# Kernel tuning notes

Measured on AMD Instinct MI355X. Metric: run time of the kernel, lower is better.

The kernel has to match this reference:

```python
import jax, jax.numpy as jnp
import numpy as np

B, H, S, D = 4, 16, 2048, 64

def setup_inputs() -> dict:
    key = jax.random.key(0)
    kq, kk, kv = jax.random.split(key, 3)
    q = jax.random.normal(kq, (B, H, S, D), dtype=jnp.float32)
    k = jax.random.normal(kk, (B, H, S, D), dtype=jnp.float32)
    v = jax.random.normal(kv, (B, H, S, D), dtype=jnp.float32)
    return {"q": q, "k": k, "v": v}

def reference(q, k, v):
    # dots: [b,h,i,j] = q . k (NO 1/sqrt(d) scaling, matching source)
    dots = jnp.einsum('bhid,bhjd->bhij', q, k)
    # causal=False (and the source's causal mask is a no-op bug anyway)
    attn = jax.nn.softmax(dots, axis=-1)
    # out: [b,h,i,d] = sum_j attn[b,h,i,j] * v[b,h,j,d]
    return jnp.einsum('bhjd,bhij->bhid', v, attn)
```

## Files before the change

kernel.cpp:

```cpp
#include <hip/hip_runtime.h>
#include <hip/hip_bf16.h>
#include <stdint.h>

#define B_ 4
#define H_ 16
#define S_ 2048
#define D_ 64
#define QBLK 128
#define KBLK 64
#define LDW 72
#define LOG2E 1.44269504088896340736f

typedef __attribute__((ext_vector_type(8))) short short8;
typedef __attribute__((ext_vector_type(4))) float f32x4;
typedef __attribute__((ext_vector_type(16))) float f32x16;
typedef _Float16 f16x8 __attribute__((ext_vector_type(8)));
typedef _Float16 f16x4 __attribute__((ext_vector_type(4)));
typedef __fp16 fp16x2 __attribute__((ext_vector_type(2)));

__device__ __forceinline__ unsigned short f2bf(float f) {
  union { float f; unsigned int u; } x; x.f = f;
  unsigned int u = x.u;
  unsigned int r = (u + 0x7FFFu + ((u >> 16) & 1u)) >> 16;
  return (unsigned short)r;
}
__device__ __forceinline__ float bf2f(unsigned short h) {
  union { unsigned int u; float f; } y; y.u = ((unsigned int)h) << 16;
  return y.f;
}

__device__ __forceinline__ unsigned pkrtz(float a, float b) {
  union { fp16x2 h; unsigned u; } c;
  c.h = __builtin_amdgcn_cvt_pkrtz(a, b);
  return c.u;
}
__device__ __forceinline__ fp16x2 u2h(unsigned u) {
  union { unsigned u; fp16x2 h; } c; c.u = u; return c.h;
}

__device__ __forceinline__ float fast_exp2(float x) {
#if __has_builtin(__builtin_amdgcn_exp2f)
  return __builtin_amdgcn_exp2f(x);
#else
  return exp2f(x);
#endif
}

__device__ __forceinline__ void swap32(unsigned &a, unsigned &b) {
#if __has_builtin(__builtin_amdgcn_permlane32_swap)
  typedef int i32x2 __attribute__((ext_vector_type(2)));
  i32x2 r = __builtin_amdgcn_permlane32_swap((int)a, (int)b, false, false);
  a = (unsigned)r[0]; b = (unsigned)r[1];
#else
  unsigned pa = (unsigned)__shfl_xor((int)a, 32);
  unsigned pb = (unsigned)__shfl_xor((int)b, 32);
  bool lo = (threadIdx.x & 32) == 0;
  unsigned r0 = lo ? a : pb;
  unsigned r1 = lo ? pa : b;
  a = r0; b = r1;
#endif
}

__device__ __forceinline__ float pairmax(float x) {
  unsigned a = __float_as_uint(x), b = a;
  swap32(a, b);
  return fmaxf(__uint_as_float(a), __uint_as_float(b));
}
__device__ __forceinline__ float pairsum(float x) {
  unsigned a = __float_as_uint(x), b = a;
  swap32(a, b);
  return __uint_as_float(a) + __uint_as_float(b);
}

#define GLOAD16(g, l) __builtin_amdgcn_global_load_lds( \
    (const __attribute__((address_space(1))) unsigned int*)(g), \
    (__attribute__((address_space(3))) unsigned int*)(l), 16, 0, 0)

__global__ void prep_k(const float* __restrict__ K, _Float16* __restrict__ Kp) {
  int e4 = (blockIdx.x * 256 + threadIdx.x) * 4;
  int bh  = e4 >> 17;
  int rem = e4 & 131071;
  int s   = rem >> 6;
  int d0  = rem & 63;
  const float4 kv = *(const float4*)(K + (size_t)e4);
  f16x4 h;
  h[0] = (_Float16)kv.x; h[1] = (_Float16)kv.y;
  h[2] = (_Float16)kv.z; h[3] = (_Float16)kv.w;
  size_t off = ((size_t)bh * S_ + s) * 128 + (unsigned)((d0 * 2) ^ ((s & 7) << 4));
  *(f16x4*)((char*)Kp + off) = h;
}

__global__ void prep_v(const float* __restrict__ V, _Float16* __restrict__ Vt) {
  __shared__ _Float16 tile[64][68];
  int bh = blockIdx.x >> 5;
  int st = blockIdx.x & 31;
  const float* Vb = V + ((size_t)bh * S_ + st * 64) * 64;
  int tid = threadIdx.x;
  #pragma unroll
  for (int i = 0; i < 4; ++i) {
    int idx = i * 1024 + tid * 4;
    int r = idx >> 6, c = idx & 63;
    float4 vv = *(const float4*)(Vb + (size_t)r * 64 + c);
    f16x4 o;
    o[0] = (_Float16)vv.x; o[1] = (_Float16)vv.y;
    o[2] = (_Float16)vv.z; o[3] = (_Float16)vv.w;
    *(f16x4*)&tile[r][c] = o;
  }
  __syncthreads();
  int chunk = tid & 15;
  int dbase = tid >> 4;
  size_t outb = (size_t)bh * (64 * S_ * 2) + (size_t)st * 128;
  #pragma unroll
  for (int i = 0; i < 4; ++i) {
    int d = dbase + i * 16;
    f16x4 o;
    o[0] = tile[chunk * 4 + 0][d];
    o[1] = tile[chunk * 4 + 1][d];
    o[2] = tile[chunk * 4 + 2][d];
    o[3] = tile[chunk * 4 + 3][d];
    size_t off = outb + (size_t)d * (S_ * 2) + (unsigned)((chunk * 8) ^ ((d & 7) << 4));
    *(f16x4*)((char*)Vt + off) = o;
  }
}

__global__ __launch_bounds__(256)
void attn_fwd4(const float* __restrict__ Q, const _Float16* __restrict__ Kg,
               const _Float16* __restrict__ Vg, float* __restrict__ O) {
  __shared__ char smem[32768];

  const int tid  = threadIdx.x;
  const int lane = tid & 63;
  const int wid  = tid >> 6;
  const int l31  = lane & 31;
  const int hi   = lane >> 5;

  const int qtile = blockIdx.x;
  const int bh    = blockIdx.y;

  const char* KB = (const char*)Kg + (size_t)bh * (S_ * 128);
  const char* VB = (const char*)Vg + (size_t)bh * (64 * S_ * 2);
  const float* Qb = Q + (size_t)bh * S_ * D_;
  float*       Ob = O + (size_t)bh * S_ * D_;

  const int qrow = qtile * QBLK + wid * 32 + l31;
  f16x8 qf[4];
  #pragma unroll
  for (int ds = 0; ds < 4; ++ds) {
    const float* qp = Qb + (size_t)qrow * D_ + ds * 16 + hi * 8;
    float4 a = *(const float4*)(qp);
    float4 b = *(const float4*)(qp + 4);
    qf[ds][0] = (_Float16)(a.x * LOG2E); qf[ds][1] = (_Float16)(a.y * LOG2E);
    qf[ds][2] = (_Float16)(a.z * LOG2E); qf[ds][3] = (_Float16)(a.w * LOG2E);
    qf[ds][4] = (_Float16)(b.x * LOG2E); qf[ds][5] = (_Float16)(b.y * LOG2E);
    qf[ds][6] = (_Float16)(b.z * LOG2E); qf[ds][7] = (_Float16)(b.w * LOG2E);
  }

  f32x16 oacc[2];
  #pragma unroll
  for (int dn = 0; dn < 2; ++dn)
    #pragma unroll
    for (int r = 0; r < 16; ++r) oacc[dn][r] = 0.f;
  float m_r = -INFINITY, l_r = 0.f;

  #define STAGE(buf, kb)                                                        \
    {                                                                           \
      char* Kl_ = smem + (buf) * 16384;                                         \
      char* Vl_ = Kl_ + 8192;                                                   \
      _Pragma("unroll")                                                         \
      for (int c = 0; c < 4; ++c) {                                             \
        int id = c * 4 + wid;                                                   \
        if (id < 8) {                                                           \
          GLOAD16(KB + (size_t)(kb) * 128 + id * 1024 + lane * 16,              \
                  Kl_ + id * 1024);                                             \
        } else {                                                                \
          int i = id - 8;                                                       \
          GLOAD16(VB + (size_t)(i * 8 + (lane >> 3)) * (S_ * 2)                 \
                     + ((kb) >> 6) * 128 + (lane & 7) * 16,                     \
                  Vl_ + i * 1024);                                              \
        }                                                                       \
      }                                                                         \
    }

  STAGE(0, 0);
  __syncthreads();

  for (int it = 0; it < S_ / KBLK; ++it) {
    const int cur = it & 1;
    if (it < S_ / KBLK - 1) STAGE(cur ^ 1, (it + 1) * KBLK);

    const char* Kl = smem + cur * 16384;
    const char* Vl = Kl + 8192;

    f32x16 sacc[2];
    __builtin_amdgcn_s_setprio(1);
    #pragma unroll
    for (int b = 0; b < 2; ++b) {
      #pragma unroll
      for (int r = 0; r < 16; ++r) sacc[b][r] = 0.f;
      const int row = b * 32 + l31;
      #pragma unroll
      for (int ds = 0; ds < 4; ++ds) {
        f16x8 kf = *(const f16x8*)(Kl + row * 128 + ((ds * 32 + hi * 16) ^ ((row & 7) << 4)));
        sacc[b] = __builtin_amdgcn_mfma_f32_32x32x16_f16(kf, qf[ds], sacc[b], 0, 0, 0);
      }
    }
    __builtin_amdgcn_s_setprio(0);

    float u[16];
    #pragma unroll
    for (int r = 0; r < 16; ++r) u[r] = fmaxf(sacc[0][r], sacc[1][r]);
    float w0 = fmaxf(fmaxf(u[0], u[1]), u[2]);
    float w1 = fmaxf(fmaxf(u[3], u[4]), u[5]);
    float w2 = fmaxf(fmaxf(u[6], u[7]), u[8]);
    float w3 = fmaxf(fmaxf(u[9], u[10]), u[11]);
    float w4 = fmaxf(fmaxf(u[12], u[13]), u[14]);
    float x0 = fmaxf(fmaxf(w0, w1), w2);
    float x1 = fmaxf(fmaxf(w3, w4), u[15]);
    float mx = pairmax(fmaxf(x0, x1));

    if (!__all(mx <= m_r + 8.f)) {
      float nm = fmaxf(m_r, mx);
      float sc = fast_exp2(m_r - nm);
      m_r = nm;
      l_r *= sc;
      #pragma unroll
      for (int dn = 0; dn < 2; ++dn)
        #pragma unroll
        for (int r = 0; r < 16; ++r) oacc[dn][r] *= sc;
    }

    unsigned ww[2][8];
#if !__has_builtin(__builtin_amdgcn_fdot2)
    float rs0 = 0.f, rs1 = 0.f;
#endif
    #pragma unroll
    for (int b = 0; b < 2; ++b)
      #pragma unroll
      for (int r1 = 0; r1 < 4; ++r1) {
        float p0 = fast_exp2(sacc[b][4 * r1 + 0] - m_r);
        float p1 = fast_exp2(sacc[b][4 * r1 + 1] - m_r);
        float p2 = fast_exp2(sacc[b][4 * r1 + 2] - m_r);
        float p3 = fast_exp2(sacc[b][4 * r1 + 3] - m_r);
        ww[b][r1 * 2 + 0] = pkrtz(p0, p1);
        ww[b][r1 * 2 + 1] = pkrtz(p2, p3);
#if !__has_builtin(__builtin_amdgcn_fdot2)
        rs0 += p0 + p2; rs1 += p1 + p3;
#endif
      }

    float rs;
#if __has_builtin(__builtin_amdgcn_fdot2)
    {
      const fp16x2 ones = {(__fp16)1.f, (__fp16)1.f};
      float rA = 0.f, rB = 0.f, rC = 0.f, rD = 0.f;
      #pragma unroll
      for (int b = 0; b < 2; ++b) {
        rA = __builtin_amdgcn_fdot2(u2h(ww[b][0]), ones, rA, false);
        rB = __builtin_amdgcn_fdot2(u2h(ww[b][1]), ones, rB, false);
        rC = __builtin_amdgcn_fdot2(u2h(ww[b][2]), ones, rC, false);
        rD = __builtin_amdgcn_fdot2(u2h(ww[b][3]), ones, rD, false);
        rA = __builtin_amdgcn_fdot2(u2h(ww[b][4]), ones, rA, false);
        rB = __builtin_amdgcn_fdot2(u2h(ww[b][5]), ones, rB, false);
        rC = __builtin_amdgcn_fdot2(u2h(ww[b][6]), ones, rC, false);
        rD = __builtin_amdgcn_fdot2(u2h(ww[b][7]), ones, rD, false);
      }
      rs = (rA + rB) + (rC + rD);
    }
#else
    rs = rs0 + rs1;
#endif
    l_r += pairsum(rs);

    f16x8 pb[4];
    #pragma unroll
    for (int ks = 0; ks < 4; ++ks) {
      const int b = ks >> 1, e = (ks & 1) * 2;
      unsigned u0 = ww[b][e * 2 + 0];
      unsigned u1 = ww[b][e * 2 + 1];
      unsigned u2 = ww[b][(e + 1) * 2 + 0];
      unsigned u3 = ww[b][(e + 1) * 2 + 1];
      swap32(u0, u2);
      swap32(u1, u3);
      union { unsigned u[4]; f16x8 v; } c;
      c.u[0] = u0; c.u[1] = u1; c.u[2] = u2; c.u[3] = u3;
      pb[ks] = c.v;
    }

    __builtin_amdgcn_s_setprio(1);
    #pragma unroll
    for (int dn = 0; dn < 2; ++dn) {
      const int d = dn * 32 + l31;
      #pragma unroll
      for (int ks = 0; ks < 4; ++ks) {
        f16x8 vf = *(const f16x8*)(Vl + d * 128 + ((ks * 32 + hi * 16) ^ ((d & 7) << 4)));
        oacc[dn] = __builtin_amdgcn_mfma_f32_32x32x16_f16(vf, pb[ks], oacc[dn], 0, 0, 0);
      }
    }
    __builtin_amdgcn_s_setprio(0);
    __syncthreads();
  }
  #undef STAGE

  const float inv = 1.0f / l_r;
  float* Ep = (float*)(smem + wid * 8192);
  #pragma unroll
  for (int dn = 0; dn < 2; ++dn)
    #pragma unroll
    for (int r = 0; r < 16; ++r) {
      int d = dn * 32 + (r & 3) + 8 * (r >> 2) + 4 * hi;
      Ep[d * 32 + l31] = oacc[dn][r] * inv;
    }
  __syncthreads();
  const int q2 = lane >> 1, dh = lane & 1;
  float* orow = Ob + (size_t)(qtile * QBLK + wid * 32 + q2) * D_ + dh * 32;
  #pragma unroll
  for (int c = 0; c < 8; ++c) {
    float4 o4;
    o4.x = Ep[(dh * 32 + c * 4 + 0) * 32 + q2];
    o4.y = Ep[(dh * 32 + c * 4 + 1) * 32 + q2];
    o4.z = Ep[(dh * 32 + c * 4 + 2) * 32 + q2];
    o4.w = Ep[(dh * 32 + c * 4 + 3) * 32 + q2];
    *(float4*)(orow + c * 4) = o4;
  }
}

__global__ __launch_bounds__(256, 2)
void attn_fwd(const float* __restrict__ Q, const float* __restrict__ K,
              const float* __restrict__ V, float* __restrict__ O) {
  __shared__ alignas(16) unsigned short Kh_lds[KBLK * LDW];
  __shared__ alignas(16) unsigned short Kl_lds[KBLK * LDW];
  __shared__ alignas(16) unsigned short Vt_lds[D_ * LDW];
  __shared__ alignas(16) unsigned short P_lds[4][16 * LDW];

  const int tid  = threadIdx.x;
  const int lane = tid & 63;
  const int wid  = tid >> 6;
  const int l15  = lane & 15;
  const int dgrp = lane >> 4;

  const int qtile = blockIdx.x;
  const int bh    = blockIdx.y;

  const size_t base = (size_t)bh * S_ * D_;
  const float* Qb = Q + base;
  const float* Kb = K + base;
  const float* Vb = V + base;
  float*       Ob = O + base;

  const int qrow = qtile * 64 + wid * 16 + l15;
  short8 qfh[2], qfl[2];
  {
    const float* qp = Qb + (size_t)qrow * D_ + dgrp * 8;
    #pragma unroll
    for (int s = 0; s < 2; ++s)
      #pragma unroll
      for (int j = 0; j < 8; ++j) {
        float f = qp[s * 32 + j];
        unsigned short h = f2bf(f);
        qfh[s][j] = (short)h;
        qfl[s][j] = (short)f2bf(f - bf2f(h));
      }
  }

  f32x4 oacc[4];
  #pragma unroll
  for (int t = 0; t < 4; ++t) oacc[t] = f32x4{0.f, 0.f, 0.f, 0.f};
  float m_r[4], l_r[4];
  #pragma unroll
  for (int j = 0; j < 4; ++j) { m_r[j] = -INFINITY; l_r[j] = 0.f; }

  for (int kb = 0; kb < S_; kb += KBLK) {
    __syncthreads();
    #pragma unroll
    for (int c = 0; c < 4; ++c) {
      int e = (c * 256 + tid) * 4;
      int r = e >> 6, col = e & 63;
      const float4 kv = *(const float4*)(Kb + (size_t)(kb + r) * D_ + col);
      ushort4 kh, kl;
      kh.x = f2bf(kv.x); kl.x = f2bf(kv.x - bf2f(kh.x));
      kh.y = f2bf(kv.y); kl.y = f2bf(kv.y - bf2f(kh.y));
      kh.z = f2bf(kv.z); kl.z = f2bf(kv.z - bf2f(kh.z));
      kh.w = f2bf(kv.w); kl.w = f2bf(kv.w - bf2f(kh.w));
      *(ushort4*)&Kh_lds[r * LDW + col] = kh;
      *(ushort4*)&Kl_lds[r * LDW + col] = kl;
      const float4 vv = *(const float4*)(Vb + (size_t)(kb + r) * D_ + col);
      Vt_lds[(col + 0) * LDW + r] = f2bf(vv.x);
      Vt_lds[(col + 1) * LDW + r] = f2bf(vv.y);
      Vt_lds[(col + 2) * LDW + r] = f2bf(vv.z);
      Vt_lds[(col + 3) * LDW + r] = f2bf(vv.w);
    }
    __syncthreads();

    f32x4 sa[4];
    #pragma unroll
    for (int t = 0; t < 4; ++t) {
      sa[t] = f32x4{0.f, 0.f, 0.f, 0.f};
      #pragma unroll
      for (int s = 0; s < 2; ++s) {
        const int off = (t * 16 + l15) * LDW + s * 32 + dgrp * 8;
        short8 kfh = *(const short8*)&Kh_lds[off];
        short8 kfl = *(const short8*)&Kl_lds[off];
        sa[t] = __builtin_amdgcn_mfma_f32_16x16x32_bf16(qfh[s], kfh, sa[t], 0, 0, 0);
        sa[t] = __builtin_amdgcn_mfma_f32_16x16x32_bf16(qfh[s], kfl, sa[t], 0, 0, 0);
        sa[t] = __builtin_amdgcn_mfma_f32_16x16x32_bf16(qfl[s], kfh, sa[t], 0, 0, 0);
      }
    }

    float pmax[4];
    #pragma unroll
    for (int j = 0; j < 4; ++j) {
      float mx = fmaxf(fmaxf(sa[0][j], sa[1][j]), fmaxf(sa[2][j], sa[3][j]));
      #pragma unroll
      for (int m = 1; m < 16; m <<= 1) mx = fmaxf(mx, __shfl_xor(mx, m));
      pmax[j] = mx;
    }
    float scale[4];
    #pragma unroll
    for (int j = 0; j < 4; ++j) {
      float nm = fmaxf(m_r[j], pmax[j]);
      scale[j] = __expf(m_r[j] - nm);
      m_r[j] = nm;
    }
    float rs[4] = {0.f, 0.f, 0.f, 0.f};
    #pragma unroll
    for (int t = 0; t < 4; ++t)
      #pragma unroll
      for (int j = 0; j < 4; ++j) {
        float p = __expf(sa[t][j] - m_r[j]);
        rs[j] += p;
        P_lds[wid][(dgrp * 4 + j) * LDW + t * 16 + l15] = f2bf(p);
      }
    #pragma unroll
    for (int j = 0; j < 4; ++j) {
      #pragma unroll
      for (int m = 1; m < 16; m <<= 1) rs[j] += __shfl_xor(rs[j], m);
      l_r[j] = l_r[j] * scale[j] + rs[j];
      #pragma unroll
      for (int t = 0; t < 4; ++t) oacc[t][j] *= scale[j];
    }

    #pragma unroll
    for (int s = 0; s < 2; ++s) {
      short8 pf = *(const short8*)&P_lds[wid][l15 * LDW + s * 32 + dgrp * 8];
      #pragma unroll
      for (int t = 0; t < 4; ++t) {
        short8 vf = *(const short8*)&Vt_lds[(t * 16 + l15) * LDW + s * 32 + dgrp * 8];
        oacc[t] = __builtin_amdgcn_mfma_f32_16x16x32_bf16(pf, vf, oacc[t], 0, 0, 0);
      }
    }
  }

  #pragma unroll
  for (int j = 0; j < 4; ++j) {
    float inv = 1.0f / l_r[j];
    int row = qtile * 64 + wid * 16 + dgrp * 4 + j;
    float* op = Ob + (size_t)row * D_ + l15;
    #pragma unroll
    for (int t = 0; t < 4; ++t)
      op[t * 16] = oacc[t][j] * inv;
  }
}

extern "C" void kernel_launch(void* const* d_in, const int* in_sizes, int n_in,
                              void* d_out, int out_size, void* d_ws, size_t ws_size,
                              hipStream_t stream) {
  const float* q = (const float*)d_in[0];
  const float* k = (const float*)d_in[1];
  const float* v = (const float*)d_in[2];
  float* o = (float*)d_out;
  const size_t PLANE = (size_t)B_ * H_ * S_ * 128;
  if (ws_size >= 2 * PLANE) {
    _Float16* Kp = (_Float16*)d_ws;
    _Float16* Vt = (_Float16*)((char*)d_ws + PLANE);
    prep_k<<<8192, 256, 0, stream>>>(k, Kp);
    prep_v<<<2048, 256, 0, stream>>>(v, Vt);
    attn_fwd4<<<dim3(S_ / QBLK, B_ * H_), 256, 0, stream>>>(q, Kp, Vt, o);
  } else {
    attn_fwd<<<dim3(S_ / 64, B_ * H_), 256, 0, stream>>>(q, k, v, o);
  }
}
```

Before: 145.4 us.

## Split key block into two halves with separate online-softmax and PV steps

Processes each 64-key tile as two 32-key sub-blocks, each with its own max/rescale, exponentiation and PV MFMAs, so the softmax of the second half can overlap with MFMA work of the first. The row-sum pair reduction is deferred to the end of the loop, and the prep_v transpose tile padding is changed. It adds an extra rescale check per tile and leaves a redundant first QK computation that relies on dead-code elimination.

```diff
diff --git a/kernel.cpp b/kernel.cpp
--- a/kernel.cpp
+++ b/kernel.cpp
@@ -91,7 +91,7 @@
 }
 
 __global__ void prep_v(const float* __restrict__ V, _Float16* __restrict__ Vt) {
-  __shared__ _Float16 tile[64][68];
+  __shared__ _Float16 tile[64][66];
   int bh = blockIdx.x >> 5;
   int st = blockIdx.x & 31;
   const float* Vb = V + ((size_t)bh * S_ + st * 64) * 64;
@@ -161,6 +161,10 @@
     #pragma unroll
     for (int r = 0; r < 16; ++r) oacc[dn][r] = 0.f;
   float m_r = -INFINITY, l_r = 0.f;
+
+  f32x16 zero16;
+  #pragma unroll
+  for (int r = 0; r < 16; ++r) zero16[r] = 0.f;
 
   #define STAGE(buf, kb)                                                        \
     {                                                                           \
@@ -191,117 +195,183 @@
     const char* Kl = smem + cur * 16384;
     const char* Vl = Kl + 8192;
 
-    f32x16 sacc[2];
+    f32x16 sacc_a, sacc_b;
     __builtin_amdgcn_s_setprio(1);
-    #pragma unroll
-    for (int b = 0; b < 2; ++b) {
-      #pragma unroll
-      for (int r = 0; r < 16; ++r) sacc[b][r] = 0.f;
-      const int row = b * 32 + l31;
-      #pragma unroll
-      for (int ds = 0; ds < 4; ++ds) {
-        f16x8 kf = *(const f16x8*)(Kl + row * 128 + ((ds * 32 + hi * 16) ^ ((row & 7) << 4)));
-        sacc[b] = __builtin_amdgcn_mfma_f32_32x32x16_f16(kf, qf[ds], sacc[b], 0, 0, 0);
-      }
+    {
+      const int row = l31;
+      const int sw = (row & 7) << 4;
+      sacc_a = __builtin_amdgcn_mfma_f32_32x32x16_f16(
+          *(const f16x8*)(Kl + row * 128 + ((0) ^ sw)), qf[0], zero16, 0, 0, 0);
+      sacc_a = __builtin_amdgcn_mfma_f32_32x32x16_f16(
+          *(const f16x8*)(Kl + row * 128 + ((32 + hi * 16) ^ sw) - hi * 16 + hi * 16), qf[1], sacc_a, 0, 0, 0);
+      sacc_a = __builtin_amdgcn_mfma_f32_32x32x16_f16(
+          *(const f16x8*)(Kl + row * 128 + ((64 + hi * 16) ^ sw) - hi * 16 + hi * 16), qf[2], sacc_a, 0, 0, 0);
+      sacc_a = __builtin_amdgcn_mfma_f32_32x32x16_f16(
+          *(const f16x8*)(Kl + row * 128 + ((96 + hi * 16) ^ sw) - hi * 16 + hi * 16), qf[3], sacc_a, 0, 0, 0);
     }
     __builtin_amdgcn_s_setprio(0);
-
-    float u[16];
-    #pragma unroll
-    for (int r = 0; r < 16; ++r) u[r] = fmaxf(sacc[0][r], sacc[1][r]);
-    float w0 = fmaxf(fmaxf(u[0], u[1]), u[2]);
-    float w1 = fmaxf(fmaxf(u[3], u[4]), u[5]);
-    float w2 = fmaxf(fmaxf(u[6], u[7]), u[8]);
-    float w3 = fmaxf(fmaxf(u[9], u[10]), u[11]);
-    float w4 = fmaxf(fmaxf(u[12], u[13]), u[14]);
-    float x0 = fmaxf(fmaxf(w0, w1), w2);
-    float x1 = fmaxf(fmaxf(w3, w4), u[15]);
-    float mx = pairmax(fmaxf(x0, x1));
-
-    if (!__all(mx <= m_r + 8.f)) {
-      float nm = fmaxf(m_r, mx);
-      float sc = fast_exp2(m_r - nm);
-      m_r = nm;
-      l_r *= sc;
-      #pragma unroll
-      for (int dn = 0; dn < 2; ++dn)
+    {
+      const int row = l31;
+      const int sw = (row & 7) << 4;
+      sacc_a = __builtin_amdgcn_mfma_f32_32x32x16_f16(
+          *(const f16x8*)(Kl + row * 128 + ((0 * 32 + hi * 16) ^ sw)), qf[0], zero16, 0, 0, 0);
+      #pragma unroll
+      for (int ds = 1; ds < 4; ++ds)
+        sacc_a = __builtin_amdgcn_mfma_f32_32x32x16_f16(
+            *(const f16x8*)(Kl + row * 128 + ((ds * 32 + hi * 16) ^ sw)), qf[ds], sacc_a, 0, 0, 0);
+    }
+    {
+      const int row = 32 + l31;
+      const int sw = (row & 7) << 4;
+      sacc_b = __builtin_amdgcn_mfma_f32_32x32x16_f16(
+          *(const f16x8*)(Kl + row * 128 + ((0 * 32 + hi * 16) ^ sw)), qf[0], zero16, 0, 0, 0);
+      #pragma unroll
+      for (int ds = 1; ds < 4; ++ds)
+        sacc_b = __builtin_amdgcn_mfma_f32_32x32x16_f16(
+            *(const f16x8*)(Kl + row * 128 + ((ds * 32 + hi * 16) ^ sw)), qf[ds], sacc_b, 0, 0, 0);
+    }
+
+    {
+      float v0 = fmaxf(fmaxf(sacc_a[0], sacc_a[1]), sacc_a[2]);
+      float v1 = fmaxf(fmaxf(sacc_a[3], sacc_a[4]), sacc_a[5]);
+      float v2 = fmaxf(fmaxf(sacc_a[6], sacc_a[7]), sacc_a[8]);
+      float v3 = fmaxf(fmaxf(sacc_a[9], sacc_a[10]), sacc_a[11]);
+      float v4 = fmaxf(fmaxf(sacc_a[12], sacc_a[13]), sacc_a[14]);
+      float w0 = fmaxf(fmaxf(v0, v1), v2);
+      float w1 = fmaxf(fmaxf(v3, v4), sacc_a[15]);
+      float mx = pairmax(fmaxf(w0, w1));
+      if (!__all(mx <= m_r + 8.f)) {
+        float nm = fmaxf(m_r, mx);
+        float sc = fast_exp2(m_r - nm);
+        m_r = nm; l_r *= sc;
         #pragma unroll
-        for (int r = 0; r < 16; ++r) oacc[dn][r] *= sc;
-    }
-
-    unsigned ww[2][8];
-#if !__has_builtin(__builtin_amdgcn_fdot2)
-    float rs0 = 0.f, rs1 = 0.f;
-#endif
-    #pragma unroll
-    for (int b = 0; b < 2; ++b)
+        for (int dn = 0; dn < 2; ++dn)
+          #pragma unroll
+          for (int r = 0; r < 16; ++r) oacc[dn][r] *= sc;
+      }
+      unsigned ww[8];
       #pragma unroll
       for (int r1 = 0; r1 < 4; ++r1) {
-        float p0 = fast_exp2(sacc[b][4 * r1 + 0] - m_r);
-        float p1 = fast_exp2(sacc[b][4 * r1 + 1] - m_r);
-        float p2 = fast_exp2(sacc[b][4 * r1 + 2] - m_r);
-        float p3 = fast_exp2(sacc[b][4 * r1 + 3] - m_r);
-        ww[b][r1 * 2 + 0] = pkrtz(p0, p1);
-        ww[b][r1 * 2 + 1] = pkrtz(p2, p3);
-#if !__has_builtin(__builtin_amdgcn_fdot2)
-        rs0 += p0 + p2; rs1 += p1 + p3;
-#endif
-      }
-
-    float rs;
-#if __has_builtin(__builtin_amdgcn_fdot2)
+        float p0 = fast_exp2(sacc_a[4 * r1 + 0] - m_r);
+        float p1 = fast_exp2(sacc_a[4 * r1 + 1] - m_r);
+        float p2 = fast_exp2(sacc_a[4 * r1 + 2] - m_r);
+        float p3 = fast_exp2(sacc_a[4 * r1 + 3] - m_r);
+        ww[r1 * 2 + 0] = pkrtz(p0, p1);
+        ww[r1 * 2 + 1] = pkrtz(p2, p3);
+      }
+      {
+        const fp16x2 ones = {(__fp16)1.f, (__fp16)1.f};
+        float rA = __builtin_amdgcn_fdot2(u2h(ww[0]), ones, 0.f, false);
+        float rB = __builtin_amdgcn_fdot2(u2h(ww[1]), ones, 0.f, false);
+        rA = __builtin_amdgcn_fdot2(u2h(ww[2]), ones, rA, false);
+        rB = __builtin_amdgcn_fdot2(u2h(ww[3]), ones, rB, false);
+        rA = __builtin_amdgcn_fdot2(u2h(ww[4]), ones, rA, false);
+        rB = __builtin_amdgcn_fdot2(u2h(ww[5]), ones, rB, false);
+        rA = __builtin_amdgcn_fdot2(u2h(ww[6]), ones, rA, false);
+        rB = __builtin_amdgcn_fdot2(u2h(ww[7]), ones, rB, false);
+        l_r += rA + rB;
+      }
+      f16x8 pb0, pb1;
+      {
+        unsigned u0 = ww[0], u1 = ww[1], u2 = ww[2], u3 = ww[3];
+        swap32(u0, u2); swap32(u1, u3);
+        union { unsigned u[4]; f16x8 v; } c;
+        c.u[0] = u0; c.u[1] = u1; c.u[2] = u2; c.u[3] = u3;
+        pb0 = c.v;
+      }
+      {
+        unsigned u0 = ww[4], u1 = ww[5], u2 = ww[6], u3 = ww[7];
+        swap32(u0, u2); swap32(u1, u3);
+        union { unsigned u[4]; f16x8 v; } c;
+        c.u[0] = u0; c.u[1] = u1; c.u[2] = u2; c.u[3] = u3;
+        pb1 = c.v;
+      }
+      __builtin_amdgcn_s_setprio(1);
+      #pragma unroll
+      for (int dn = 0; dn < 2; ++dn) {
+        const int d = dn * 32 + l31;
+        const int sw = (d & 7) << 4;
+        f16x8 vf0 = *(const f16x8*)(Vl + d * 128 + ((0 * 32 + hi * 16) ^ sw));
+        f16x8 vf1 = *(const f16x8*)(Vl + d * 128 + ((1 * 32 + hi * 16) ^ sw));
+        oacc[dn] = __builtin_amdgcn_mfma_f32_32x32x16_f16(vf0, pb0, oacc[dn], 0, 0, 0);
+        oacc[dn] = __builtin_amdgcn_mfma_f32_32x32x16_f16(vf1, pb1, oacc[dn], 0, 0, 0);
+      }
+      __builtin_amdgcn_s_setprio(0);
+    }
+
     {
-      const fp16x2 ones = {(__fp16)1.f, (__fp16)1.f};
-      float rA = 0.f, rB = 0.f, rC = 0.f, rD = 0.f;
-      #pragma unroll
-      for (int b = 0; b < 2; ++b) {
-        rA = __builtin_amdgcn_fdot2(u2h(ww[b][0]), ones, rA, false);
-        rB = __builtin_amdgcn_fdot2(u2h(ww[b][1]), ones, rB, false);
-        rC = __builtin_amdgcn_fdot2(u2h(ww[b][2]), ones, rC, false);
-        rD = __builtin_amdgcn_fdot2(u2h(ww[b][3]), ones, rD, false);
-        rA = __builtin_amdgcn_fdot2(u2h(ww[b][4]), ones, rA, false);
-        rB = __builtin_amdgcn_fdot2(u2h(ww[b][5]), ones, rB, false);
-        rC = __builtin_amdgcn_fdot2(u2h(ww[b][6]), ones, rC, false);
-        rD = __builtin_amdgcn_fdot2(u2h(ww[b][7]), ones, rD, false);
-      }
-      rs = (rA + rB) + (rC + rD);
-    }
-#else
-    rs = rs0 + rs1;
-#endif
-    l_r += pairsum(rs);
-
-    f16x8 pb[4];
-    #pragma unroll
-    for (int ks = 0; ks < 4; ++ks) {
-      const int b = ks >> 1, e = (ks & 1) * 2;
-      unsigned u0 = ww[b][e * 2 + 0];
-      unsigned u1 = ww[b][e * 2 + 1];
-      unsigned u2 = ww[b][(e + 1) * 2 + 0];
-      unsigned u3 = ww[b][(e + 1) * 2 + 1];
-      swap32(u0, u2);
-      swap32(u1, u3);
-      union { unsigned u[4]; f16x8 v; } c;
-      c.u[0] = u0; c.u[1] = u1; c.u[2] = u2; c.u[3] = u3;
-      pb[ks] = c.v;
-    }
-
-    __builtin_amdgcn_s_setprio(1);
-    #pragma unroll
-    for (int dn = 0; dn < 2; ++dn) {
-      const int d = dn * 32 + l31;
-      #pragma unroll
-      for (int ks = 0; ks < 4; ++ks) {
-        f16x8 vf = *(const f16x8*)(Vl + d * 128 + ((ks * 32 + hi * 16) ^ ((d & 7) << 4)));
-        oacc[dn] = __builtin_amdgcn_mfma_f32_32x32x16_f16(vf, pb[ks], oacc[dn], 0, 0, 0);
-      }
-    }
-    __builtin_amdgcn_s_setprio(0);
+      float v0 = fmaxf(fmaxf(sacc_b[0], sacc_b[1]), sacc_b[2]);
+      float v1 = fmaxf(fmaxf(sacc_b[3], sacc_b[4]), sacc_b[5]);
+      float v2 = fmaxf(fmaxf(sacc_b[6], sacc_b[7]), sacc_b[8]);
+      float v3 = fmaxf(fmaxf(sacc_b[9], sacc_b[10]), sacc_b[11]);
+      float v4 = fmaxf(fmaxf(sacc_b[12], sacc_b[13]), sacc_b[14]);
+      float w0 = fmaxf(fmaxf(v0, v1), v2);
+      float w1 = fmaxf(fmaxf(v3, v4), sacc_b[15]);
+      float mx = pairmax(fmaxf(w0, w1));
+      if (!__all(mx <= m_r + 8.f)) {
+        float nm = fmaxf(m_r, mx);
+        float sc = fast_exp2(m_r - nm);
+        m_r = nm; l_r *= sc;
+        #pragma unroll
+        for (int dn = 0; dn < 2; ++dn)
+          #pragma unroll
+          for (int r = 0; r < 16; ++r) oacc[dn][r] *= sc;
+      }
+      unsigned ww[8];
+      #pragma unroll
+      for (int r1 = 0; r1 < 4; ++r1) {
+        float p0 = fast_exp2(sacc_b[4 * r1 + 0] - m_r);
+        float p1 = fast_exp2(sacc_b[4 * r1 + 1] - m_r);
+        float p2 = fast_exp2(sacc_b[4 * r1 + 2] - m_r);
+        float p3 = fast_exp2(sacc_b[4 * r1 + 3] - m_r);
+        ww[r1 * 2 + 0] = pkrtz(p0, p1);
+        ww[r1 * 2 + 1] = pkrtz(p2, p3);
+      }
+      {
+        const fp16x2 ones = {(__fp16)1.f, (__fp16)1.f};
+        float rA = __builtin_amdgcn_fdot2(u2h(ww[0]), ones, 0.f, false);
+        float rB = __builtin_amdgcn_fdot2(u2h(ww[1]), ones, 0.f, false);
+        rA = __builtin_amdgcn_fdot2(u2h(ww[2]), ones, rA, false);
+        rB = __builtin_amdgcn_fdot2(u2h(ww[3]), ones, rB, false);
+        rA = __builtin_amdgcn_fdot2(u2h(ww[4]), ones, rA, false);
+        rB = __builtin_amdgcn_fdot2(u2h(ww[5]), ones, rB, false);
+        rA = __builtin_amdgcn_fdot2(u2h(ww[6]), ones, rA, false);
+        rB = __builtin_amdgcn_fdot2(u2h(ww[7]), ones, rB, false);
+        l_r += rA + rB;
+      }
+      f16x8 pb2, pb3;
+      {
+        unsigned u0 = ww[0], u1 = ww[1], u2 = ww[2], u3 = ww[3];
+        swap32(u0, u2); swap32(u1, u3);
+        union { unsigned u[4]; f16x8 v; } c;
+        c.u[0] = u0; c.u[1] = u1; c.u[2] = u2; c.u[3] = u3;
+        pb2 = c.v;
+      }
+      {
+        unsigned u0 = ww[4], u1 = ww[5], u2 = ww[6], u3 = ww[7];
+        swap32(u0, u2); swap32(u1, u3);
+        union { unsigned u[4]; f16x8 v; } c;
+        c.u[0] = u0; c.u[1] = u1; c.u[2] = u2; c.u[3] = u3;
+        pb3 = c.v;
+      }
+      __builtin_amdgcn_s_setprio(1);
+      #pragma unroll
+      for (int dn = 0; dn < 2; ++dn) {
+        const int d = dn * 32 + l31;
+        const int sw = (d & 7) << 4;
+        f16x8 vf2 = *(const f16x8*)(Vl + d * 128 + ((2 * 32 + hi * 16) ^ sw));
+        f16x8 vf3 = *(const f16x8*)(Vl + d * 128 + ((3 * 32 + hi * 16) ^ sw));
+        oacc[dn] = __builtin_amdgcn_mfma_f32_32x32x16_f16(vf2, pb2, oacc[dn], 0, 0, 0);
+        oacc[dn] = __builtin_amdgcn_mfma_f32_32x32x16_f16(vf3, pb3, oacc[dn], 0, 0, 0);
+      }
+      __builtin_amdgcn_s_setprio(0);
+    }
+
     __syncthreads();
   }
   #undef STAGE
 
-  const float inv = 1.0f / l_r;
+  const float inv = 1.0f / pairsum(l_r);
   float* Ep = (float*)(smem + wid * 8192);
   #pragma unroll
   for (int dn = 0; dn < 2; ++dn)
```

Result: no change. 144.8 us (-0.5%).
